# Kernel tuning notes

Measured on AMD Instinct MI355X. Metric: run time of the kernel, lower is better.

## Reference

```python
import jax, jax.numpy as jnp
import numpy as np

N, E, F, H, G = 50000, 1600000, 128, 128, 64
EPS = 1e-5  # BatchNorm eps


def setup_inputs() -> dict:
    key = jax.random.key(0)
    ks = jax.random.split(key, 16)
    x = jax.random.normal(ks[0], (N, F), dtype=jnp.float32)
    edge_index = jax.random.randint(ks[1], (2, E), 0, N, dtype=jnp.int64)
    batch = jnp.sort(jax.random.randint(ks[2], (N,), 0, G, dtype=jnp.int64))
    inp = {
        'x': x, 'edge_index': edge_index, 'batch': batch,
        'W1': jax.random.normal(ks[3], (F, H), dtype=jnp.float32) / np.sqrt(F),
        'b1': jnp.zeros((H,), jnp.float32),
        'bn1_gamma': jax.random.uniform(ks[4], (H,), jnp.float32, 0.5, 1.5),
        'bn1_beta': jax.random.normal(ks[5], (H,), jnp.float32) * 0.1,
        'bn1_mean': jax.random.normal(ks[6], (H,), jnp.float32) * 0.1,
        'bn1_var': jax.random.uniform(ks[7], (H,), jnp.float32, 0.5, 1.5),
        'W2': jax.random.normal(ks[8], (H, H), dtype=jnp.float32) / np.sqrt(H),
        'b2': jnp.zeros((H,), jnp.float32),
        'bn2_gamma': jax.random.uniform(ks[9], (H,), jnp.float32, 0.5, 1.5),
        'bn2_beta': jax.random.normal(ks[10], (H,), jnp.float32) * 0.1,
        'bn2_mean': jax.random.normal(ks[11], (H,), jnp.float32) * 0.1,
        'bn2_var': jax.random.uniform(ks[12], (H,), jnp.float32, 0.5, 1.5),
        'att_w': jax.random.normal(ks[13], (H, 1), dtype=jnp.float32) / np.sqrt(H),
        'cls_w': jax.random.normal(ks[14], (1, H), dtype=jnp.float32) / np.sqrt(H),
        'cls_b': jnp.zeros((1,), jnp.float32),
    }
    return inp


def gcn_conv(h, W, b, src, dst, n):
    # PyG GCNConv: linear, add self-loops, symmetric D^{-1/2}(A+I)D^{-1/2} aggregation, bias.
    hw = h @ W                                   # [n, H]
    loops = jnp.arange(n, dtype=src.dtype)
    s = jnp.concatenate([src, loops])
    d = jnp.concatenate([dst, loops])
    deg = jax.ops.segment_sum(jnp.ones_like(d, dtype=hw.dtype), d, num_segments=n)
    dis = jnp.where(deg > 0, jax.lax.rsqrt(deg), 0.0)
    norm = dis[s] * dis[d]                       # [E+n]
    msgs = hw[s] * norm[:, None]                 # gather + scale (memory-bound)
    return jax.ops.segment_sum(msgs, d, num_segments=n) + b


def batch_norm(h, gamma, beta, mean, var):
    return (h - mean) * gamma * jax.lax.rsqrt(var + EPS) + beta


def reference(x, edge_index, batch, W1, b1, bn1_gamma, bn1_beta, bn1_mean, bn1_var,
              W2, b2, bn2_gamma, bn2_beta, bn2_mean, bn2_var, att_w, cls_w, cls_b):
    n = x.shape[0]
    src, dst = edge_index[0], edge_index[1]
    # eval mode: dropout and edge-dropout are no-ops; BN uses running stats
    h = gcn_conv(x, W1, b1, src, dst, n)
    h = jax.nn.relu(batch_norm(h, bn1_gamma, bn1_beta, bn1_mean, bn1_var))
    h = gcn_conv(h, W2, b2, src, dst, n)
    h = jax.nn.relu(batch_norm(h, bn2_gamma, bn2_beta, bn2_mean, bn2_var))
    att = jax.nn.sigmoid(h @ att_w)              # [n, 1]
    g = jax.ops.segment_sum(h * att, batch, num_segments=G)  # [G, H]
    logits = g @ cls_w.T + cls_b                 # [G, 1]
    return logits, att
```

## Files before the change

kernel.cpp:

```cpp
#include <hip/hip_runtime.h>
#include <math.h>

#define NN 50000
#define HID 128
#define NG 64
#define BN_EPS 1e-5f

typedef __attribute__((ext_vector_type(8))) short short8;
typedef __attribute__((ext_vector_type(4))) float f32x4;
typedef __attribute__((ext_vector_type(2))) float f32x2;

__device__ inline unsigned pack_bf2(float a, float b) {
    union { float f; unsigned u; } ua, ub;
    ua.f = a; ub.f = b;
    unsigned x = ua.u, y = ub.u;
    x += 0x7fffu + ((x >> 16) & 1u);
    y += 0x7fffu + ((y >> 16) & 1u);
    return (x >> 16) | (y & 0xffff0000u);
}
__device__ inline unsigned short bf16_1(float x) {
    union { float f; unsigned u; } v;
    v.f = x;
    unsigned r = v.u + 0x7fffu + ((v.u >> 16) & 1u);
    return (unsigned short)(r >> 16);
}
__device__ inline float2 unpack_bf2(unsigned v) {
    union { unsigned u; float f; } a, b;
    a.u = v << 16;
    b.u = v & 0xffff0000u;
    return make_float2(a.f, b.f);
}
__device__ __forceinline__ f32x2 bf2_to_f32x2(unsigned u) {
    union { unsigned q; float f; } a, b;
    a.q = u << 16;
    b.q = u & 0xffff0000u;
    f32x2 r;
    r.x = a.f;
    r.y = b.f;
    return r;
}

#define NBKT 256
#define ETILE 4096
#define EPT   (ETILE / 256)
#define CAP   10240
#define ASTR 136

__global__ __launch_bounds__(128) void k_prep0(const float* __restrict__ W1,
                                               const float* __restrict__ W2,
                                               unsigned short* __restrict__ wt1,
                                               unsigned short* __restrict__ wt2,
                                               int* __restrict__ bcurP,
                                               const float* __restrict__ cls_b,
                                               float* __restrict__ logits) {
    int b = blockIdx.x;
    int t = threadIdx.x;
    if (b < 256) {
        int k = b & 127;
        const float* W = (b < 128) ? W1 : W2;
        unsigned short* wt = (b < 128) ? wt1 : wt2;
        wt[t * 128 + k] = bf16_1(W[k * 128 + t]);
    } else {
        #pragma unroll
        for (int i = 0; i < 32; ++i) bcurP[t * 32 + i] = 0;
        if (t < NG) logits[t] = cls_b[0];
    }
}

__device__ __forceinline__ void gemm1_tile(char* smem, int row0,
                                           const float* __restrict__ x,
                                           const unsigned short* __restrict__ wt1,
                                           unsigned short* __restrict__ zb,
                                           int n, int t) {
    typedef unsigned short ArowT[ASTR];
    ArowT* A = (ArowT*)smem;
    #pragma unroll
    for (int i = 0; i < 8; ++i) {
        int idx = t + i * 256;
        int r = idx >> 5;
        int c4 = (idx & 31) * 4;
        float4 v = make_float4(0.f, 0.f, 0.f, 0.f);
        if (row0 + r < n) v = *(const float4*)&x[(size_t)(row0 + r) * 128 + c4];
        uint2 p;
        p.x = pack_bf2(v.x, v.y);
        p.y = pack_bf2(v.z, v.w);
        *(uint2*)&A[r][c4] = p;
    }
    __syncthreads();
    int lane = t & 63;
    int wave = t >> 6;
    int m = lane & 15;
    int quad = lane >> 4;
    int r0 = wave * 16;
    short8 a[4];
    #pragma unroll
    for (int kt = 0; kt < 4; ++kt)
        a[kt] = *(const short8*)&A[r0 + m][kt * 32 + quad * 8];
    f32x4 acc[8];
    #pragma unroll
    for (int ct = 0; ct < 8; ++ct) acc[ct] = (f32x4){0.f, 0.f, 0.f, 0.f};
    short8 bcur[4], bnxt[4];
    {
        const unsigned short* wb = &wt1[(size_t)m * 128 + quad * 8];
        #pragma unroll
        for (int kt = 0; kt < 4; ++kt) bcur[kt] = *(const short8*)(wb + kt * 32);
    }
    #pragma unroll
    for (int ct = 0; ct < 8; ++ct) {
        if (ct < 7) {
            const unsigned short* wb = &wt1[(size_t)((ct + 1) * 16 + m) * 128 + quad * 8];
            #pragma unroll
            for (int kt = 0; kt < 4; ++kt) bnxt[kt] = *(const short8*)(wb + kt * 32);
        }
        #pragma unroll
        for (int kt = 0; kt < 4; ++kt)
            acc[ct] = __builtin_amdgcn_mfma_f32_16x16x32_bf16(a[kt], bcur[kt], acc[ct], 0, 0, 0);
        #pragma unroll
        for (int kt = 0; kt < 4; ++kt) bcur[kt] = bnxt[kt];
    }
    __syncthreads();
    #pragma unroll
    for (int ct = 0; ct < 8; ++ct) {
        int col = ct * 16 + m;
        #pragma unroll
        for (int reg = 0; reg < 4; ++reg)
            A[r0 + quad * 4 + reg][col] = bf16_1(acc[ct][reg]);
    }
    __syncthreads();
    #pragma unroll
    for (int i = 0; i < 4; ++i) {
        int idx = t + i * 256;
        int r = idx >> 4;
        int c8 = (idx & 15) * 8;
        int grow = row0 + r;
        if (grow < n)
            *(uint4*)&zb[(size_t)grow * 128 + c8] = *(const uint4*)&A[r][c8];
    }
}

struct SmemDist {
    int h[NBKT], sx[NBKT], cur[NBKT], gb[NBKT];
    unsigned stage[ETILE];
};

__global__ __launch_bounds__(256) void k_dist_gemm1(const int* __restrict__ src,
                                                    const int* __restrict__ dst,
                                                    int* __restrict__ bcurP,
                                                    unsigned* __restrict__ bpacked,
                                                    const float* __restrict__ x,
                                                    const unsigned short* __restrict__ wt1,
                                                    unsigned short* __restrict__ zb,
                                                    int E, int n, int DB) {
    __shared__ __align__(16) char smem[sizeof(SmemDist)];
    int t = threadIdx.x;
    int b = blockIdx.x;

    if (b >= DB) {
        gemm1_tile(smem, (b - DB) * 64, x, wt1, zb, n, t);
        return;
    }
    SmemDist* s = (SmemDist*)smem;
    s->h[t] = 0;
    __syncthreads();
    int base = b * ETILE;
    int dreg[EPT];
    #pragma unroll
    for (int i = 0; i < EPT; ++i) {
        int e = base + i * 256 + t;
        dreg[i] = (e < E) ? dst[e] : -1;
        if (dreg[i] >= 0) atomicAdd(&s->h[dreg[i] >> 8], 1);
    }
    __syncthreads();
    int c = s->h[t];
    s->sx[t] = c;
    __syncthreads();
    for (int off = 1; off < NBKT; off <<= 1) {
        int v = (t >= off) ? s->sx[t - off] : 0;
        __syncthreads();
        s->sx[t] += v;
        __syncthreads();
    }
    int nvalid = s->sx[NBKT - 1];
    int excl = s->sx[t] - c;
    __syncthreads();
    s->sx[t] = excl;
    s->cur[t] = excl;
    s->gb[t] = (c > 0) ? atomicAdd(&bcurP[t * 16], c) : 0;
    __syncthreads();
    #pragma unroll
    for (int i = 0; i < EPT; ++i) {
        int e = base + i * 256 + t;
        if (dreg[i] >= 0) {
            int d = dreg[i];
            int bkt = d >> 8;
            int p = atomicAdd(&s->cur[bkt], 1);
            s->stage[p] = ((unsigned)d << 16) | (unsigned)src[e];
        }
    }
    __syncthreads();
    for (int idx = t; idx < nvalid; idx += 256) {
        unsigned v = s->stage[idx];
        int bkt = (int)(v >> 24);
        int pos = s->gb[bkt] + (idx - s->sx[bkt]);
        bpacked[(size_t)bkt * CAP + pos] = v;
    }
}

struct SmemCSR {
    int cnt[NBKT], sA[NBKT], cur[NBKT];
    unsigned short stage[CAP];
};

__global__ __launch_bounds__(256) void k_csr_gemm1(const unsigned* __restrict__ bpacked,
                                                   const int* __restrict__ bcurP,
                                                   int* __restrict__ row_ptr,
                                                   int* __restrict__ degA,
                                                   float* __restrict__ dis,
                                                   unsigned short* __restrict__ col16,
                                                   const float* __restrict__ x,
                                                   const unsigned short* __restrict__ wt1,
                                                   unsigned short* __restrict__ zb,
                                                   int n, int NB, int row0B) {
    __shared__ __align__(16) char smem[sizeof(SmemCSR)];
    int t = threadIdx.x;
    int b = blockIdx.x;

    if (b >= NB) {
        gemm1_tile(smem, row0B + (b - NB) * 64, x, wt1, zb, n, t);
        return;
    }
    SmemCSR* s = (SmemCSR*)smem;
    int node0 = b << 8;
    int nn = n - node0;
    if (nn > 256) nn = 256;
    if (nn < 0) nn = 0;
    int e0 = b * CAP;
    int ne = bcurP[b * 16];
    s->cnt[t] = 0;
    __syncthreads();
    int n4 = (ne + 3) >> 2;
    for (int i = t; i < n4; i += 256) {
        uint4 v = *(const uint4*)&bpacked[e0 + 4 * i];
        int rem = ne - 4 * i;
        if (rem > 0) atomicAdd(&s->cnt[(v.x >> 16) & 255u], 1);
        if (rem > 1) atomicAdd(&s->cnt[(v.y >> 16) & 255u], 1);
        if (rem > 2) atomicAdd(&s->cnt[(v.z >> 16) & 255u], 1);
        if (rem > 3) atomicAdd(&s->cnt[(v.w >> 16) & 255u], 1);
    }
    __syncthreads();
    int c = s->cnt[t];
    s->sA[t] = c;
    __syncthreads();
    for (int off = 1; off < NBKT; off <<= 1) {
        int v = (t >= off) ? s->sA[t - off] : 0;
        __syncthreads();
        s->sA[t] += v;
        __syncthreads();
    }
    int excl = s->sA[t] - c;
    s->cur[t] = excl;
    if (t < nn) {
        row_ptr[node0 + t] = e0 + excl;
        degA[node0 + t] = c;
        dis[node0 + t] = rsqrtf((float)(c + 1));
    }
    __syncthreads();
    for (int i = t; i < n4; i += 256) {
        uint4 v = *(const uint4*)&bpacked[e0 + 4 * i];
        int rem = ne - 4 * i;
        unsigned vv[4] = {v.x, v.y, v.z, v.w};
        #pragma unroll
        for (int j = 0; j < 4; ++j) {
            if (rem > j) {
                int ld = (int)((vv[j] >> 16) & 255u);
                int p = atomicAdd(&s->cur[ld], 1);
                s->stage[p] = (unsigned short)(vv[j] & 0xFFFFu);
            }
        }
    }
    __syncthreads();
    int nw = (ne + 1) >> 1;
    for (int i = t; i < nw; i += 256) {
        unsigned w = (unsigned)s->stage[2 * i] | ((unsigned)s->stage[2 * i + 1] << 16);
        *(unsigned*)&col16[e0 + 2 * i] = w;
    }
}

__global__ __launch_bounds__(256) void k_scale(unsigned short* __restrict__ zb,
                                               const float* __restrict__ dis, int n) {
    int i = blockIdx.x * 256 + threadIdx.x;
    int r = i >> 4;
    if (r >= n) return;
    int c8 = (i & 15) * 8;
    float s = dis[r];
    uint4 v = *(const uint4*)&zb[(size_t)r * 128 + c8];
    unsigned* w = (unsigned*)&v;
    #pragma unroll
    for (int k = 0; k < 4; ++k) {
        float2 f = unpack_bf2(w[k]);
        w[k] = pack_bf2(f.x * s, f.y * s);
    }
    *(uint4*)&zb[(size_t)r * 128 + c8] = v;
}


__device__ __forceinline__ void consume8(const uint4* v, f32x2* acc) {
    #pragma unroll
    for (int j = 0; j < 8; ++j) {
        const unsigned* w = (const unsigned*)&v[j];
        #pragma unroll
        for (int i2 = 0; i2 < 4; ++i2)
            acc[i2] += bf2_to_f32x2(w[i2]);
    }
}

__device__ __forceinline__ void gather_pipe(const unsigned short* __restrict__ hws,
                                            const unsigned short* __restrict__ col16,
                                            int e0, int deg, int md, int sl, int part,
                                            f32x2* acc) {
    int nt = (md + 7) >> 3;
    if (nt <= 0) return;
    int base = part << 4;
    uint4 vA[8], vB[8];
    int c0, c1, n0 = 0, n1 = 0;
    c0 = (sl < deg) ? (int)col16[e0 + sl] : 0;
    c1 = (sl + 16 < deg) ? (int)col16[e0 + 16 + sl] : 0;

    #pragma unroll
    for (int j = 0; j < 8; ++j) {
        int s = __shfl(c0, base + j);
        vA[j] = (j < deg) ? *(const uint4*)(hws + ((size_t)s << 7) + (sl << 3))
                          : make_uint4(0, 0, 0, 0);
    }
    int t = 0, ebase = 0;
    for (;;) {
        if (t + 4 < nt) {
            n0 = (ebase + 32 + sl < deg) ? (int)col16[e0 + ebase + 32 + sl] : 0;
            n1 = (ebase + 48 + sl < deg) ? (int)col16[e0 + ebase + 48 + sl] : 0;
        }
        if (t + 1 < nt) {
            int it0 = (t + 1) << 3;
            #pragma unroll
            for (int j = 0; j < 8; ++j) {
                int s = __shfl(c0, base + 8 + j);
                vB[j] = (it0 + j < deg) ? *(const uint4*)(hws + ((size_t)s << 7) + (sl << 3))
                                        : make_uint4(0, 0, 0, 0);
            }
        }
        consume8(vA, acc);
        if (++t >= nt) break;
        if (t + 1 < nt) {
            int it0 = (t + 1) << 3;
            #pragma unroll
            for (int j = 0; j < 8; ++j) {
                int s = __shfl(c1, base + j);
                vA[j] = (it0 + j < deg) ? *(const uint4*)(hws + ((size_t)s << 7) + (sl << 3))
                                        : make_uint4(0, 0, 0, 0);
            }
        }
        consume8(vB, acc);
        if (++t >= nt) break;
        if (t + 1 < nt) {
            int it0 = (t + 1) << 3;
            #pragma unroll
            for (int j = 0; j < 8; ++j) {
                int s = __shfl(c1, base + 8 + j);
                vB[j] = (it0 + j < deg) ? *(const uint4*)(hws + ((size_t)s << 7) + (sl << 3))
                                        : make_uint4(0, 0, 0, 0);
            }
        }
        consume8(vA, acc);
        if (++t >= nt) break;
        if (t + 1 < nt) {
            int it0 = (t + 1) << 3;
            #pragma unroll
            for (int j = 0; j < 8; ++j) {
                int s = __shfl(n0, base + j);
                vA[j] = (it0 + j < deg) ? *(const uint4*)(hws + ((size_t)s << 7) + (sl << 3))
                                        : make_uint4(0, 0, 0, 0);
            }
        }
        consume8(vB, acc);
        if (++t >= nt) break;
        c0 = n0; c1 = n1; ebase += 32;
    }
}


__global__ __launch_bounds__(256, 3) void k_agg1_gemm2(const unsigned short* __restrict__ zb,
                                                       const int* __restrict__ row_ptr,
                                                       const int* __restrict__ degA,
                                                       const unsigned short* __restrict__ col16,
                                                       const float* __restrict__ dis,
                                                       const float* __restrict__ bias,
                                                       const float* __restrict__ gamma,
                                                       const float* __restrict__ beta,
                                                       const float* __restrict__ mean,
                                                       const float* __restrict__ var,
                                                       const unsigned short* __restrict__ wt2,
                                                       unsigned short* __restrict__ hwsb2, int n) {
    __shared__ unsigned short H1[16][ASTR];
    __shared__ unsigned short C2[16][ASTR];
    int t = threadIdx.x;
    int wave = t >> 6, lane = t & 63;
    int sl = lane & 15, part = lane >> 4;
    int d = blockIdx.x * 16 + wave * 4 + part;
    bool active = (d < n);
    int e0 = 0, deg = 0;
    if (active) {
        e0 = row_ptr[d];
        deg = degA[d];
    }
    uint4 vs = make_uint4(0, 0, 0, 0);
    float dd = 0.f;
    if (active) {
        vs = *(const uint4*)(zb + ((size_t)d << 7) + (sl << 3));
        dd = dis[d];
    }
    int md = deg;
    md = max(md, __shfl_xor(md, 16));
    md = max(md, __shfl_xor(md, 32));

    f32x2 acc[4];
    #pragma unroll
    for (int i = 0; i < 4; ++i) acc[i] = (f32x2){0.f, 0.f};
    gather_pipe(zb, col16, e0, deg, md, sl, part, acc);

    unsigned outw[4] = {0, 0, 0, 0};
    if (active) {
        const unsigned* w = (const unsigned*)&vs;
        #pragma unroll
        for (int i2 = 0; i2 < 4; ++i2)
            acc[i2] += bf2_to_f32x2(w[i2]);
        int f0 = sl << 3;
        #pragma unroll
        for (int i2 = 0; i2 < 4; ++i2) {
            int f = f0 + 2 * i2;
            float2 bv = *(const float2*)&bias[f];
            float2 gm = *(const float2*)&gamma[f];
            float2 bt = *(const float2*)&beta[f];
            float2 mn = *(const float2*)&mean[f];
            float2 vr = *(const float2*)&var[f];
            float vx = acc[i2].x * dd + bv.x;
            float vy = acc[i2].y * dd + bv.y;
            float sx = gm.x * rsqrtf(vr.x + BN_EPS);
            float sy = gm.y * rsqrtf(vr.y + BN_EPS);
            float rx = fmaxf((vx - mn.x) * sx + bt.x, 0.f);
            float ry = fmaxf((vy - mn.y) * sy + bt.y, 0.f);
            outw[i2] = pack_bf2(rx, ry);
        }
    }
    int local = wave * 4 + part;
    *(uint4*)&H1[local][sl << 3] = *(uint4*)outw;
    __syncthreads();

    int m = sl;
    int quad = part;
    short8 a2[4];
    #pragma unroll
    for (int kt = 0; kt < 4; ++kt)
        a2[kt] = *(const short8*)&H1[m][kt * 32 + quad * 8];

    f32x4 acc2[2];
    acc2[0] = (f32x4){0.f, 0.f, 0.f, 0.f};
    acc2[1] = (f32x4){0.f, 0.f, 0.f, 0.f};
    #pragma unroll
    for (int i = 0; i < 2; ++i) {
        int ct = wave * 2 + i;
        const unsigned short* wb = &wt2[(size_t)(ct * 16 + m) * 128 + quad * 8];
        #pragma unroll
        for (int kt = 0; kt < 4; ++kt) {
            short8 b = *(const short8*)(wb + kt * 32);
            acc2[i] = __builtin_amdgcn_mfma_f32_16x16x32_bf16(a2[kt], b, acc2[i], 0, 0, 0);
        }
    }
    int gr = blockIdx.x * 16 + quad * 4;
    float ds2[4];
    #pragma unroll
    for (int reg = 0; reg < 4; ++reg)
        ds2[reg] = (gr + reg < n) ? dis[gr + reg] : 0.f;
    #pragma unroll
    for (int i = 0; i < 2; ++i) {
        int col = (wave * 2 + i) * 16 + m;
        #pragma unroll
        for (int reg = 0; reg < 4; ++reg)
            C2[quad * 4 + reg][col] = bf16_1(acc2[i][reg] * ds2[reg]);
    }
    __syncthreads();
    {
        int r = t >> 4;
        int c8 = (t & 15) * 8;
        int grow = blockIdx.x * 16 + r;
        if (grow < n)
            *(uint4*)&hwsb2[(size_t)grow * 128 + c8] = *(const uint4*)&C2[r][c8];
    }
}


__global__ __launch_bounds__(256, 3) void k_agg2_att_logit(const unsigned short* __restrict__ hwsb,
                                                           const int* __restrict__ row_ptr,
                                                           const int* __restrict__ degA,
                                                           const unsigned short* __restrict__ col16,
                                                           const float* __restrict__ dis,
                                                           const float* __restrict__ bias,
                                                           const float* __restrict__ gamma,
                                                           const float* __restrict__ beta,
                                                           const float* __restrict__ mean,
                                                           const float* __restrict__ var,
                                                           const int* __restrict__ batch,
                                                           const float* __restrict__ att_w,
                                                           const float* __restrict__ cls_w,
                                                           float* __restrict__ att_out,
                                                           float* __restrict__ logits, int n) {
    __shared__ int   sg[16];
    __shared__ float sv[16];
    int t = threadIdx.x;
    int wave = t >> 6, lane = t & 63;
    int sl = lane & 15, part = lane >> 4;
    int d = blockIdx.x * 16 + wave * 4 + part;
    bool active = (d < n);
    int e0 = 0, deg = 0;
    if (active) {
        e0 = row_ptr[d];
        deg = degA[d];
    }
    uint4 vs = make_uint4(0, 0, 0, 0);
    float dd = 0.f;
    int g = -1;
    if (active) {
        vs = *(const uint4*)(hwsb + ((size_t)d << 7) + (sl << 3));
        dd = dis[d];
        g = batch[d];
    }
    int md = deg;
    md = max(md, __shfl_xor(md, 16));
    md = max(md, __shfl_xor(md, 32));

    f32x2 acc[4];
    #pragma unroll
    for (int i = 0; i < 4; ++i) acc[i] = (f32x2){0.f, 0.f};
    gather_pipe(hwsb, col16, e0, deg, md, sl, part, acc);

    float contrib = 0.f;
    float p = 0.f, q = 0.f;
    if (active) {
        const unsigned* w = (const unsigned*)&vs;
        #pragma unroll
        for (int i2 = 0; i2 < 4; ++i2)
            acc[i2] += bf2_to_f32x2(w[i2]);
        float dd2 = dd;
        int f0 = sl << 3;
        #pragma unroll
        for (int i2 = 0; i2 < 4; ++i2) {
            int f = f0 + 2 * i2;
            float2 bv = *(const float2*)&bias[f];
            float2 gm = *(const float2*)&gamma[f];
            float2 bt = *(const float2*)&beta[f];
            float2 mn = *(const float2*)&mean[f];
            float2 vr = *(const float2*)&var[f];
            float vx = acc[i2].x * dd2 + bv.x;
            float vy = acc[i2].y * dd2 + bv.y;
            float sx = gm.x * rsqrtf(vr.x + BN_EPS);
            float sy = gm.y * rsqrtf(vr.y + BN_EPS);
            float rx = fmaxf((vx - mn.x) * sx + bt.x, 0.f);
            float ry = fmaxf((vy - mn.y) * sy + bt.y, 0.f);
            float2 aw = *(const float2*)&att_w[f];
            float2 cw = *(const float2*)&cls_w[f];
            p += rx * aw.x + ry * aw.y;
            q += rx * cw.x + ry * cw.y;
        }
    }
    #pragma unroll
    for (int off = 1; off < 16; off <<= 1) {
        p += __shfl_xor(p, off);
        q += __shfl_xor(q, off);
    }
    if (active) {
        float a = 1.f / (1.f + expf(-p));
        if (sl == 0) att_out[d] = a;
        contrib = a * q;
    }
    if (sl == 0) {
        sg[wave * 4 + part] = g;
        sv[wave * 4 + part] = contrib;
    }
    __syncthreads();
    if (t == 0) {
        int cur = -1;
        float acc2 = 0.f;
        #pragma unroll
        for (int i = 0; i < 16; ++i) {
            int gi = sg[i];
            if (gi < 0) continue;
            if (gi != cur) {
                if (cur >= 0) atomicAdd(&logits[cur], acc2);
                cur = gi;
                acc2 = 0.f;
            }
            acc2 += sv[i];
        }
        if (cur >= 0) atomicAdd(&logits[cur], acc2);
    }
}


extern "C" void kernel_launch(void* const* d_in, const int* in_sizes, int n_in,
                              void* d_out, int out_size, void* d_ws, size_t ws_size,
                              hipStream_t stream) {
    const float* x   = (const float*)d_in[0];
    const int*   ei  = (const int*)d_in[1];
    const int*   bat = (const int*)d_in[2];
    const float* W1  = (const float*)d_in[3];
    const float* b1  = (const float*)d_in[4];
    const float* g1  = (const float*)d_in[5];
    const float* bt1 = (const float*)d_in[6];
    const float* mn1 = (const float*)d_in[7];
    const float* vr1 = (const float*)d_in[8];
    const float* W2  = (const float*)d_in[9];
    const float* b2  = (const float*)d_in[10];
    const float* g2  = (const float*)d_in[11];
    const float* bt2 = (const float*)d_in[12];
    const float* mn2 = (const float*)d_in[13];
    const float* vr2 = (const float*)d_in[14];
    const float* attw = (const float*)d_in[15];
    const float* clsw = (const float*)d_in[16];
    const float* clsb = (const float*)d_in[17];

    int E = in_sizes[1] / 2;
    int n = in_sizes[2];
    const int* src = ei;
    const int* dst = ei + E;
    int NB = (n + 255) >> 8;

    char* ws = (char*)d_ws;
    auto alloc = [&](size_t bytes) {
        void* p = (void*)ws;
        ws += (bytes + 255) & ~(size_t)255;
        return p;
    };
    int*            bcurP   = (int*)alloc(NBKT * 16 * 4);
    unsigned*       bpacked = (unsigned*)alloc((size_t)NBKT * CAP * 4);
    int*            row_ptr = (int*)alloc((size_t)n * 4);
    int*            degA    = (int*)alloc((size_t)n * 4);
    unsigned short* col16   = (unsigned short*)alloc(((size_t)NBKT * CAP + 1024) * 2);
    float*          dis     = (float*)alloc((size_t)n * 4);
    unsigned short* zb      = (unsigned short*)alloc((size_t)n * 128 * 2);
    unsigned short* hwsb2   = (unsigned short*)alloc((size_t)n * 128 * 2);
    unsigned short* wt1     = (unsigned short*)alloc(128 * 128 * 2);
    unsigned short* wt2     = (unsigned short*)alloc(128 * 128 * 2);

    float* out = (float*)d_out;
    int DB = (E + ETILE - 1) / ETILE;
    int gb = (n + 63) / 64;
    int G1A = gb / 2;
    int G1B = gb - G1A;
    int ab = (n + 15) / 16;
    int sb = (n * 16 + 255) / 256;

    k_prep0<<<257, 128, 0, stream>>>(W1, W2, wt1, wt2, bcurP, clsb, out);
    k_dist_gemm1<<<DB + G1A, 256, 0, stream>>>(src, dst, bcurP, bpacked, x, wt1, zb,
                                               E, n, DB);
    k_csr_gemm1<<<NB + G1B, 256, 0, stream>>>(bpacked, bcurP, row_ptr, degA, dis,
                                              col16, x, wt1, zb, n, NB, G1A * 64);
    k_scale<<<sb, 256, 0, stream>>>(zb, dis, n);
    k_agg1_gemm2<<<ab, 256, 0, stream>>>(zb, row_ptr, degA, col16, dis,
                                         b1, g1, bt1, mn1, vr1, wt2, hwsb2, n);
    k_agg2_att_logit<<<ab, 256, 0, stream>>>(hwsb2, row_ptr, degA, col16, dis,
                                             b2, g2, bt2, mn2, vr2, bat, attw, clsw,
                                             out + NG, out, n);
}
```

Baseline: 256.9 us.

## Pad CSR rows to group-max multiple of eight with zero-row sentinel

Builds the CSR with each node's row padded to the maximum degree among each group of four nodes, rounded up to a multiple of eight. Padding entries point to an extra all-zero row at index n in both feature buffers. This lets the gather pipeline drop its per-edge bounds checks and conditional loads. In exchange it adds redundant loads of the zero row, a larger column buffer, and extra shared-memory staging and fill work in the CSR build kernel.

```diff
diff --git a/kernel.cpp b/kernel.cpp
--- a/kernel.cpp
+++ b/kernel.cpp
@@ -43,7 +43,8 @@
 #define NBKT 256
 #define ETILE 4096
 #define EPT   (ETILE / 256)
-#define CAP   10240
+#define CAPB  10240
+#define CAPC  12800
 #define ASTR 136
 
 __global__ __launch_bounds__(128) void k_prep0(const float* __restrict__ W1,
@@ -52,7 +53,10 @@
                                                unsigned short* __restrict__ wt2,
                                                int* __restrict__ bcurP,
                                                const float* __restrict__ cls_b,
-                                               float* __restrict__ logits) {
+                                               float* __restrict__ logits,
+                                               unsigned short* __restrict__ zb,
+                                               unsigned short* __restrict__ hwsb2,
+                                               int n) {
     int b = blockIdx.x;
     int t = threadIdx.x;
     if (b < 256) {
@@ -64,6 +68,8 @@
         #pragma unroll
         for (int i = 0; i < 32; ++i) bcurP[t * 32 + i] = 0;
         if (t < NG) logits[t] = cls_b[0];
+        if (t < 64) *(unsigned*)((char*)zb + (size_t)n * 256 + t * 4) = 0u;
+        else        *(unsigned*)((char*)hwsb2 + (size_t)n * 256 + (t - 64) * 4) = 0u;
     }
 }
 
@@ -202,13 +208,13 @@
         unsigned v = s->stage[idx];
         int bkt = (int)(v >> 24);
         int pos = s->gb[bkt] + (idx - s->sx[bkt]);
-        bpacked[(size_t)bkt * CAP + pos] = v;
+        bpacked[(size_t)bkt * CAPB + pos] = v;
     }
 }
 
 struct SmemCSR {
     int cnt[NBKT], sA[NBKT], cur[NBKT];
-    unsigned short stage[CAP];
+    unsigned short stage[CAPC];
 };
 
 __global__ __launch_bounds__(256) void k_csr_gemm1(const unsigned* __restrict__ bpacked,
@@ -234,7 +240,8 @@
     int nn = n - node0;
     if (nn > 256) nn = 256;
     if (nn < 0) nn = 0;
-    int e0 = b * CAP;
+    int e0 = b * CAPB;
+    int e0c = b * CAPC;
     int ne = bcurP[b * 16];
     s->cnt[t] = 0;
     __syncthreads();
@@ -249,7 +256,10 @@
     }
     __syncthreads();
     int c = s->cnt[t];
-    s->sA[t] = c;
+    int gm = max(c, __shfl_xor(c, 1));
+    gm = max(gm, __shfl_xor(gm, 2));
+    int P = (gm + 7) & ~7;
+    s->sA[t] = P;
     __syncthreads();
     for (int off = 1; off < NBKT; off <<= 1) {
         int v = (t >= off) ? s->sA[t - off] : 0;
@@ -257,13 +267,17 @@
         s->sA[t] += v;
         __syncthreads();
     }
-    int excl = s->sA[t] - c;
+    int excl = s->sA[t] - P;
     s->cur[t] = excl;
     if (t < nn) {
-        row_ptr[node0 + t] = e0 + excl;
-        degA[node0 + t] = c;
+        row_ptr[node0 + t] = e0c + excl;
+        degA[node0 + t] = P;
         dis[node0 + t] = rsqrtf((float)(c + 1));
     }
+    __syncthreads();
+    int totP = s->sA[NBKT - 1];
+    unsigned short sent = (unsigned short)n;
+    for (int i = t; i < totP; i += 256) s->stage[i] = sent;
     __syncthreads();
     for (int i = t; i < n4; i += 256) {
         uint4 v = *(const uint4*)&bpacked[e0 + 4 * i];
@@ -279,10 +293,10 @@
         }
     }
     __syncthreads();
-    int nw = (ne + 1) >> 1;
+    int nw = totP >> 1;
     for (int i = t; i < nw; i += 256) {
         unsigned w = (unsigned)s->stage[2 * i] | ((unsigned)s->stage[2 * i + 1] << 16);
-        *(unsigned*)&col16[e0 + 2 * i] = w;
+        *(unsigned*)&col16[e0c + 2 * i] = w;
     }
 }
 
@@ -314,72 +328,44 @@
     }
 }
 
+__device__ __forceinline__ void issue8(const unsigned short* __restrict__ hws,
+                                       int sl, int lsel, int creg, uint4* v) {
+    #pragma unroll
+    for (int j = 0; j < 8; ++j) {
+        int s = __shfl(creg, lsel + j);
+        v[j] = *(const uint4*)(hws + ((size_t)s << 7) + (sl << 3));
+    }
+}
+
 __device__ __forceinline__ void gather_pipe(const unsigned short* __restrict__ hws,
                                             const unsigned short* __restrict__ col16,
-                                            int e0, int deg, int md, int sl, int part,
+                                            int e0, int P, int sl, int part,
                                             f32x2* acc) {
-    int nt = (md + 7) >> 3;
+    int nt = P >> 3;
     if (nt <= 0) return;
     int base = part << 4;
     uint4 vA[8], vB[8];
-    int c0, c1, n0 = 0, n1 = 0;
-    c0 = (sl < deg) ? (int)col16[e0 + sl] : 0;
-    c1 = (sl + 16 < deg) ? (int)col16[e0 + 16 + sl] : 0;
-
-    #pragma unroll
-    for (int j = 0; j < 8; ++j) {
-        int s = __shfl(c0, base + j);
-        vA[j] = (j < deg) ? *(const uint4*)(hws + ((size_t)s << 7) + (sl << 3))
-                          : make_uint4(0, 0, 0, 0);
-    }
+    int c0 = (int)col16[e0 + sl];
+    int c1 = (int)col16[e0 + 16 + sl];
+    int n0 = 0, n1 = 0;
+
+    issue8(hws, sl, base, c0, vA);
     int t = 0, ebase = 0;
     for (;;) {
         if (t + 4 < nt) {
-            n0 = (ebase + 32 + sl < deg) ? (int)col16[e0 + ebase + 32 + sl] : 0;
-            n1 = (ebase + 48 + sl < deg) ? (int)col16[e0 + ebase + 48 + sl] : 0;
-        }
-        if (t + 1 < nt) {
-            int it0 = (t + 1) << 3;
-            #pragma unroll
-            for (int j = 0; j < 8; ++j) {
-                int s = __shfl(c0, base + 8 + j);
-                vB[j] = (it0 + j < deg) ? *(const uint4*)(hws + ((size_t)s << 7) + (sl << 3))
-                                        : make_uint4(0, 0, 0, 0);
-            }
-        }
+            n0 = (int)col16[e0 + ebase + 32 + sl];
+            n1 = (int)col16[e0 + ebase + 48 + sl];
+        }
+        if (t + 1 < nt) issue8(hws, sl, base + 8, c0, vB);
         consume8(vA, acc);
         if (++t >= nt) break;
-        if (t + 1 < nt) {
-            int it0 = (t + 1) << 3;
-            #pragma unroll
-            for (int j = 0; j < 8; ++j) {
-                int s = __shfl(c1, base + j);
-                vA[j] = (it0 + j < deg) ? *(const uint4*)(hws + ((size_t)s << 7) + (sl << 3))
-                                        : make_uint4(0, 0, 0, 0);
-            }
-        }
+        if (t + 1 < nt) issue8(hws, sl, base, c1, vA);
         consume8(vB, acc);
         if (++t >= nt) break;
-        if (t + 1 < nt) {
-            int it0 = (t + 1) << 3;
-            #pragma unroll
-            for (int j = 0; j < 8; ++j) {
-                int s = __shfl(c1, base + 8 + j);
-                vB[j] = (it0 + j < deg) ? *(const uint4*)(hws + ((size_t)s << 7) + (sl << 3))
-                                        : make_uint4(0, 0, 0, 0);
-            }
-        }
+        if (t + 1 < nt) issue8(hws, sl, base + 8, c1, vB);
         consume8(vA, acc);
         if (++t >= nt) break;
-        if (t + 1 < nt) {
-            int it0 = (t + 1) << 3;
-            #pragma unroll
-            for (int j = 0; j < 8; ++j) {
-                int s = __shfl(n0, base + j);
-                vA[j] = (it0 + j < deg) ? *(const uint4*)(hws + ((size_t)s << 7) + (sl << 3))
-                                        : make_uint4(0, 0, 0, 0);
-            }
-        }
+        if (t + 1 < nt) issue8(hws, sl, base, n0, vA);
         consume8(vB, acc);
         if (++t >= nt) break;
         c0 = n0; c1 = n1; ebase += 32;
@@ -406,10 +392,10 @@
     int sl = lane & 15, part = lane >> 4;
     int d = blockIdx.x * 16 + wave * 4 + part;
     bool active = (d < n);
-    int e0 = 0, deg = 0;
+    int e0 = 0, P = 0;
     if (active) {
         e0 = row_ptr[d];
-        deg = degA[d];
+        P = degA[d];
     }
     uint4 vs = make_uint4(0, 0, 0, 0);
     float dd = 0.f;
@@ -417,14 +403,14 @@
         vs = *(const uint4*)(zb + ((size_t)d << 7) + (sl << 3));
         dd = dis[d];
     }
-    int md = deg;
+    int md = P;
     md = max(md, __shfl_xor(md, 16));
     md = max(md, __shfl_xor(md, 32));
 
     f32x2 acc[4];
     #pragma unroll
     for (int i = 0; i < 4; ++i) acc[i] = (f32x2){0.f, 0.f};
-    gather_pipe(zb, col16, e0, deg, md, sl, part, acc);
+    gather_pipe(zb, col16, e0, md, sl, part, acc);
 
     unsigned outw[4] = {0, 0, 0, 0};
     if (active) {
@@ -519,10 +505,10 @@
     int sl = lane & 15, part = lane >> 4;
     int d = blockIdx.x * 16 + wave * 4 + part;
     bool active = (d < n);
-    int e0 = 0, deg = 0;
+    int e0 = 0, P = 0;
     if (active) {
         e0 = row_ptr[d];
-        deg = degA[d];
+        P = degA[d];
     }
     uint4 vs = make_uint4(0, 0, 0, 0);
     float dd = 0.f;
@@ -532,14 +518,14 @@
         dd = dis[d];
         g = batch[d];
     }
-    int md = deg;
+    int md = P;
     md = max(md, __shfl_xor(md, 16));
     md = max(md, __shfl_xor(md, 32));
 
     f32x2 acc[4];
     #pragma unroll
     for (int i = 0; i < 4; ++i) acc[i] = (f32x2){0.f, 0.f};
-    gather_pipe(hwsb, col16, e0, deg, md, sl, part, acc);
+    gather_pipe(hwsb, col16, e0, md, sl, part, acc);
 
     float contrib = 0.f;
     float p = 0.f, q = 0.f;
@@ -639,13 +625,13 @@
         return p;
     };
     int*            bcurP   = (int*)alloc(NBKT * 16 * 4);
-    unsigned*       bpacked = (unsigned*)alloc((size_t)NBKT * CAP * 4);
+    unsigned*       bpacked = (unsigned*)alloc((size_t)NBKT * CAPB * 4);
     int*            row_ptr = (int*)alloc((size_t)n * 4);
     int*            degA    = (int*)alloc((size_t)n * 4);
-    unsigned short* col16   = (unsigned short*)alloc(((size_t)NBKT * CAP + 1024) * 2);
+    unsigned short* col16   = (unsigned short*)alloc(((size_t)NBKT * CAPC + 1024) * 2);
     float*          dis     = (float*)alloc((size_t)n * 4);
-    unsigned short* zb      = (unsigned short*)alloc((size_t)n * 128 * 2);
-    unsigned short* hwsb2   = (unsigned short*)alloc((size_t)n * 128 * 2);
+    unsigned short* zb      = (unsigned short*)alloc((size_t)(n + 1) * 128 * 2);
+    unsigned short* hwsb2   = (unsigned short*)alloc((size_t)(n + 1) * 128 * 2);
     unsigned short* wt1     = (unsigned short*)alloc(128 * 128 * 2);
     unsigned short* wt2     = (unsigned short*)alloc(128 * 128 * 2);
 
@@ -657,7 +643,7 @@
     int ab = (n + 15) / 16;
     int sb = (n * 16 + 255) / 256;
 
-    k_prep0<<<257, 128, 0, stream>>>(W1, W2, wt1, wt2, bcurP, clsb, out);
+    k_prep0<<<257, 128, 0, stream>>>(W1, W2, wt1, wt2, bcurP, clsb, out, zb, hwsb2, n);
     k_dist_gemm1<<<DB + G1A, 256, 0, stream>>>(src, dst, bcurP, bpacked, x, wt1, zb,
                                                E, n, DB);
     k_csr_gemm1<<<NB + G1B, 256, 0, stream>>>(bpacked, bcurP, row_ptr, degA, dis,
```

Measured after the change: 255.3 us. About the same (-0.6%).
